# Kernel tuning notes

Measured on AMD Instinct MI355X. Metric: run time of the kernel, lower is better.

## Reference

```python
import jax, jax.numpy as jnp
import numpy as np

B, S, D, H = 2, 2048, 1024, 16
DH = D // H
DFF = 4 * D
EPS = 1e-5


def layer_norm(x, w, b):
    m = jnp.mean(x, axis=-1, keepdims=True)
    v = jnp.mean((x - m) ** 2, axis=-1, keepdims=True)
    return (x - m) / jnp.sqrt(v + EPS) * w + b


def setup_inputs() -> dict:
    key = jax.random.key(0)
    ks = jax.random.split(key, 12)
    s = 0.02
    x = jax.random.normal(ks[0], (B, S, D), dtype=jnp.float32)
    mask = jnp.tril(jnp.ones((S, S), dtype=jnp.int32))  # causal mask, 0 = blocked
    Wq = jax.random.normal(ks[1], (H, D, DH), dtype=jnp.float32) * s
    Wk = jax.random.normal(ks[2], (H, D, DH), dtype=jnp.float32) * s
    Wv = jax.random.normal(ks[3], (H, D, DH), dtype=jnp.float32) * s
    Wo = jax.random.normal(ks[4], (D, D), dtype=jnp.float32) * s
    bo = jnp.zeros((D,), dtype=jnp.float32)
    W1 = jax.random.normal(ks[5], (D, DFF), dtype=jnp.float32) * s
    b1 = jnp.zeros((DFF,), dtype=jnp.float32)
    W2 = jax.random.normal(ks[6], (DFF, D), dtype=jnp.float32) * s
    b2 = jnp.zeros((D,), dtype=jnp.float32)
    ln1_w = jnp.ones((D,), dtype=jnp.float32)
    ln1_b = jnp.zeros((D,), dtype=jnp.float32)
    ln2_w = jnp.ones((D,), dtype=jnp.float32)
    ln2_b = jnp.zeros((D,), dtype=jnp.float32)
    return {"x": x, "mask": mask, "Wq": Wq, "Wk": Wk, "Wv": Wv, "Wo": Wo,
            "bo": bo, "W1": W1, "b1": b1, "W2": W2, "b2": b2,
            "ln1_w": ln1_w, "ln1_b": ln1_b, "ln2_w": ln2_w, "ln2_b": ln2_b}


def reference(x, mask, Wq, Wk, Wv, Wo, bo, W1, b1, W2, b2,
              ln1_w, ln1_b, ln2_w, ln2_b):
    # --- pre-LN attention ---
    xn = layer_norm(x, ln1_w, ln1_b)
    q = jnp.einsum('bsd,hdk->bhsk', xn, Wq)  # [B,H,S,DH]
    k = jnp.einsum('bsd,hdk->bhsk', xn, Wk)
    v = jnp.einsum('bsd,hdk->bhsk', xn, Wv)
    scores = jnp.einsum('bhik,bhjk->bhij', q, k) / jnp.sqrt(jnp.float32(DH))
    scores = jnp.where(mask == 0, jnp.float32(-1e9), scores)  # mask broadcasts [S,S]->[B,H,S,S]
    attn = jax.nn.softmax(scores, axis=-1)
    o = jnp.einsum('bhij,bhjk->bhik', attn, v)        # [B,H,S,DH]
    o = o.transpose(0, 2, 1, 3).reshape(x.shape[0], x.shape[1], D)  # concat heads
    attn_out = o @ Wo + bo
    x = x + attn_out
    # --- pre-LN FFN ---
    xn2 = layer_norm(x, ln2_w, ln2_b)
    h = jax.nn.relu(xn2 @ W1 + b1)
    x = x + (h @ W2 + b2)
    return x
```

## Files before the change

kernel.cpp:

```cpp
#include <hip/hip_runtime.h>
#include <hip/hip_bf16.h>
#include <stdint.h>

#define DEV static __device__ __forceinline__

using f32x4  = __attribute__((ext_vector_type(4))) float;
using bf16x8 = __attribute__((ext_vector_type(8))) __bf16;

constexpr int SEQ = 2048;

DEV unsigned short f2bf(float f) {
  union { float f; unsigned u; } c; c.f = f;
  unsigned u = c.u;
  u += 0x7fffu + ((u >> 16) & 1u);
  return (unsigned short)(u >> 16);
}

DEV float wred_sum(float v) {
  #pragma unroll
  for (int m = 32; m > 0; m >>= 1) v += __shfl_xor(v, m, 64);
  return v;
}

DEV void g2l16(const unsigned short* g, unsigned short* l) {
  __builtin_amdgcn_global_load_lds(
      (const __attribute__((address_space(1))) void*)g,
      (__attribute__((address_space(3))) void*)l, 16, 0, 0);
}

DEV int xcd_map(int bid, int nwg) {
  const int cpx = nwg >> 3;
  return (bid & 7) * cpx + (bid >> 3);
}

__global__ __launch_bounds__(256) void convw_kernel(
    const float* __restrict__ in, unsigned short* __restrict__ out,
    int K, int Nh)
{
  const int h = blockIdx.z;
  const float* inh = in + (size_t)h * K * Nh;
  unsigned short* outh = out + (size_t)h * Nh * K;
  const int n0 = blockIdx.x * 32, k0 = blockIdx.y * 32;
  __shared__ float t[32][33];
  const int tx = threadIdx.x & 31, ty = threadIdx.x >> 5;
  #pragma unroll
  for (int r = 0; r < 32; r += 8)
    t[ty + r][tx] = inh[(size_t)(k0 + ty + r) * Nh + (n0 + tx)];
  __syncthreads();
  #pragma unroll
  for (int r = 0; r < 32; r += 8)
    outh[(size_t)(n0 + ty + r) * K + (k0 + tx)] = f2bf(t[tx][ty + r]);
}

__global__ __launch_bounds__(256) void ln_kernel(
    const float* __restrict__ x, const float* __restrict__ w,
    const float* __restrict__ b, unsigned short* __restrict__ out)
{
  const int row = blockIdx.x;
  const int tid = threadIdx.x;
  const float4 v = ((const float4*)(x + (size_t)row * 1024))[tid];
  float s  = v.x + v.y + v.z + v.w;
  float s2 = v.x*v.x + v.y*v.y + v.z*v.z + v.w*v.w;
  s = wred_sum(s); s2 = wred_sum(s2);
  __shared__ float rs[4], rs2[4];
  const int wave = tid >> 6, lane = tid & 63;
  if (lane == 0) { rs[wave] = s; rs2[wave] = s2; }
  __syncthreads();
  const float S  = rs[0] + rs[1] + rs[2] + rs[3];
  const float S2 = rs2[0] + rs2[1] + rs2[2] + rs2[3];
  const float mean = S * (1.f / 1024.f);
  const float var  = S2 * (1.f / 1024.f) - mean * mean;
  const float inv  = rsqrtf(var + 1e-5f);
  const float4 wv = ((const float4*)w)[tid];
  const float4 bv = ((const float4*)b)[tid];
  ushort4 o;
  o.x = f2bf((v.x - mean) * inv * wv.x + bv.x);
  o.y = f2bf((v.y - mean) * inv * wv.y + bv.y);
  o.z = f2bf((v.z - mean) * inv * wv.z + bv.z);
  o.w = f2bf((v.w - mean) * inv * wv.w + bv.w);
  ((ushort4*)(out + (size_t)row * 1024))[tid] = o;
}

template<int EPI>
__global__ __launch_bounds__(256) void gemm_kp(
    const unsigned short* __restrict__ A, const unsigned short* __restrict__ BT,
    void* __restrict__ Cout, const float* __restrict__ bias,
    const float* __restrict__ res, int M, int N, int K)
{
  __shared__ unsigned short sA[4][128 * 32];
  __shared__ unsigned short sB[4][64 * 32];
  const int tid = threadIdx.x;
  const int wave = tid >> 6, lane = tid & 63;
  const int wr = wave >> 1, wc = wave & 1;
  const int bid = xcd_map(blockIdx.y * gridDim.x + blockIdx.x, gridDim.x * gridDim.y);
  const int m0 = (bid / gridDim.x) * 128, n0 = (bid % gridDim.x) * 64;
  const int lr = lane & 15, lg = lane >> 4;
  const int wb = tid & 192;

  const f32x4 zero = {0.f, 0.f, 0.f, 0.f};
  f32x4 acc[4][2];
  #pragma unroll
  for (int i = 0; i < 4; ++i)
    #pragma unroll
    for (int j = 0; j < 2; ++j) acc[i][j] = zero;

  auto STAGE = [&](int slot, int kt) {
    const int k0 = kt * 32;
    #pragma unroll
    for (int r = 0; r < 2; ++r) {
      const int c = tid + 256 * r;
      const int row = c >> 2;
      const int so = ((c & 3) ^ ((row >> 1) & 3)) * 8;
      g2l16(A + (size_t)(m0 + row) * K + k0 + so, sA[slot] + (size_t)(r * 256 + wb) * 8);
    }
    const int row = tid >> 2;
    const int so = ((tid & 3) ^ ((row >> 1) & 3)) * 8;
    g2l16(BT + (size_t)(n0 + row) * K + k0 + so, sB[slot] + (size_t)wb * 8);
  };

  const int nt = K / 32;
  STAGE(0, 0); STAGE(1, 1); STAGE(2, 2);

  for (int t = 0; t < nt; ++t) {
    asm volatile("s_waitcnt vmcnt(6)" ::: "memory");
    __builtin_amdgcn_s_barrier();
    const int slot = t & 3;
    bf16x8 af[4], bfr[2];
    #pragma unroll
    for (int i = 0; i < 4; ++i) {
      const int row = wr * 64 + i * 16 + lr;
      af[i] = *(const bf16x8*)(sA[slot] + row * 32 + ((lg ^ ((row >> 1) & 3)) << 3));
    }
    #pragma unroll
    for (int j = 0; j < 2; ++j) {
      const int row = wc * 32 + j * 16 + lr;
      bfr[j] = *(const bf16x8*)(sB[slot] + row * 32 + ((lg ^ ((row >> 1) & 3)) << 3));
    }
    #pragma unroll
    for (int i = 0; i < 4; ++i)
      #pragma unroll
      for (int j = 0; j < 2; ++j)
        acc[i][j] = __builtin_amdgcn_mfma_f32_16x16x32_bf16(af[i], bfr[j], acc[i][j], 0, 0, 0);
    const int nx = (t + 3 < nt) ? t + 3 : nt - 1;
    STAGE((t + 3) & 3, nx);
  }
  asm volatile("s_waitcnt vmcnt(0)" ::: "memory");

  #pragma unroll
  for (int i = 0; i < 4; ++i) {
    #pragma unroll
    for (int j = 0; j < 2; ++j) {
      #pragma unroll
      for (int r = 0; r < 4; ++r) {
        const int row = m0 + wr * 64 + i * 16 + lg * 4 + r;
        const int col = n0 + wc * 32 + j * 16 + lr;
        const float v = acc[i][j][r];
        if (EPI == 1) {
          ((float*)Cout)[(size_t)row * N + col] = v + bias[col] + res[(size_t)row * N + col];
        } else {
          ((unsigned short*)Cout)[(size_t)row * N + col] = f2bf(v);
        }
      }
    }
  }
}

template<int EPI>
__global__ __launch_bounds__(512) void gemm256(
    const unsigned short* __restrict__ A, const unsigned short* __restrict__ BT,
    void* __restrict__ Cout, const float* __restrict__ bias,
    int M, int N, int K)
{
  __shared__ unsigned short sA[2][256 * 64];
  __shared__ unsigned short sB[2][256 * 64];
  const int tid = threadIdx.x;
  const int lane = tid & 63;
  const int wave = tid >> 6;
  const int wm = wave >> 2, wn = wave & 3;
  const int bid = xcd_map(blockIdx.y * gridDim.x + blockIdx.x, gridDim.x * gridDim.y);
  const int m0 = (bid / gridDim.x) * 256, n0 = (bid % gridDim.x) * 256;
  const int lr = lane & 15, lg = lane >> 4;

  const f32x4 zero = {0.f, 0.f, 0.f, 0.f};
  f32x4 acc[8][4];
  #pragma unroll
  for (int i = 0; i < 8; ++i)
    #pragma unroll
    for (int j = 0; j < 4; ++j) acc[i][j] = zero;

  auto STAGE = [&](int buf, int k0) {
    #pragma unroll
    for (int r = 0; r < 4; ++r) {
      const int c = tid + 512 * r;
      const int row = c >> 3;
      const int slot = (c & 7) ^ (row & 7);
      const int cb = (tid & 448) + 512 * r;
      g2l16(A  + (size_t)(m0 + row) * K + k0 + slot * 8, sA[buf] + (size_t)cb * 8);
      g2l16(BT + (size_t)(n0 + row) * K + k0 + slot * 8, sB[buf] + (size_t)cb * 8);
    }
  };
  auto RD = [&](const unsigned short* base, int R, int C) -> const bf16x8* {
    return (const bf16x8*)(base + R * 64 + ((((C >> 3) ^ (R & 7))) << 3));
  };

  const int nt = K / 64;
  STAGE(0, 0);
  asm volatile("s_waitcnt vmcnt(0)" ::: "memory");
  __syncthreads();

  for (int t = 0; t < nt; ++t) {
    const int buf = t & 1;
    if (t + 1 < nt) STAGE(buf ^ 1, (t + 1) * 64);
    #pragma unroll
    for (int p = 0; p < 4; ++p) {
      const int ih = p >> 1, jh = p & 1;
      bf16x8 af[4][2], bfr[2][2];
      #pragma unroll
      for (int i = 0; i < 4; ++i)
        #pragma unroll
        for (int kk = 0; kk < 2; ++kk)
          af[i][kk] = *RD(sA[buf], wm * 128 + (ih * 4 + i) * 16 + lr, kk * 32 + lg * 8);
      #pragma unroll
      for (int j = 0; j < 2; ++j)
        #pragma unroll
        for (int kk = 0; kk < 2; ++kk)
          bfr[j][kk] = *RD(sB[buf], wn * 64 + (jh * 2 + j) * 16 + lr, kk * 32 + lg * 8);
      __builtin_amdgcn_s_setprio(1);
      #pragma unroll
      for (int i = 0; i < 4; ++i)
        #pragma unroll
        for (int j = 0; j < 2; ++j)
          #pragma unroll
          for (int kk = 0; kk < 2; ++kk)
            acc[ih * 4 + i][jh * 2 + j] = __builtin_amdgcn_mfma_f32_16x16x32_bf16(
                af[i][kk], bfr[j][kk], acc[ih * 4 + i][jh * 2 + j], 0, 0, 0);
      __builtin_amdgcn_s_setprio(0);
      if (p < 3) __builtin_amdgcn_s_barrier();
    }
    asm volatile("s_waitcnt vmcnt(0)" ::: "memory");
    __builtin_amdgcn_s_barrier();
  }

  #pragma unroll
  for (int i = 0; i < 8; ++i) {
    #pragma unroll
    for (int j = 0; j < 4; ++j) {
      #pragma unroll
      for (int r = 0; r < 4; ++r) {
        const int row = m0 + wm * 128 + i * 16 + lg * 4 + r;
        const int col = n0 + wn * 64 + j * 16 + lr;
        const float v = acc[i][j][r];
        if (EPI == 0) {
          ((unsigned short*)Cout)[(size_t)row * N + col] = f2bf(v);
        } else {
          float t2 = v + bias[col];
          t2 = t2 > 0.f ? t2 : 0.f;
          ((unsigned short*)Cout)[(size_t)row * N + col] = f2bf(t2);
        }
      }
    }
  }
}

constexpr int PAD  = 72;
constexpr int VPAD = 136;

__global__ __launch_bounds__(256) void attn_mfma(
    const unsigned short* __restrict__ qkv, unsigned short* __restrict__ o)
{
  const int p  = blockIdx.x >> 5;
  const int bh = blockIdx.x & 31;
  const int b = bh >> 4, h = bh & 15;
  const int tid = threadIdx.x;
  const int wave = tid >> 6, lane = tid & 63;
  const int lr = lane & 15, lg = lane >> 4;
  const float SC = 0.125f * 1.44269504089f;

  __shared__ unsigned short Ks[128 * PAD];
  __shared__ unsigned short Vs[64 * VPAD];
  __shared__ unsigned short Ps[4][16 * VPAD];

  #pragma unroll 1
  for (int ph = 0; ph < 2; ++ph) {
    const int qi = ph ? (31 - p) : p;
    const int q0 = qi * 64;

    const size_t qbase = ((size_t)(b * SEQ + q0 + wave * 16 + lr)) * 3072 + h * 64;
    bf16x8 qb[2];
    qb[0] = *(const bf16x8*)(qkv + qbase + lg * 8);
    qb[1] = *(const bf16x8*)(qkv + qbase + 32 + lg * 8);

    const f32x4 zero = {0.f, 0.f, 0.f, 0.f};
    f32x4 o_acc[4];
    #pragma unroll
    for (int dn = 0; dn < 4; ++dn) o_acc[dn] = zero;
    float m_run = -1e30f, l_run = 0.f;

    const int ntiles = (qi + 2) >> 1;
    for (int t = 0; t < ntiles; ++t) {
      const int j0 = t * 128;
      __syncthreads();
      #pragma unroll
      for (int r = 0; r < 4; ++r) {
        const int c = tid + 256 * r;
        const int row = c >> 3, seg = c & 7;
        const size_t base = ((size_t)(b * SEQ + j0 + row)) * 3072 + 1024 + h * 64 + seg * 8;
        *(int4*)(Ks + row * PAD + seg * 8) = *(const int4*)(qkv + base);
      }
      #pragma unroll
      for (int r = 0; r < 4; ++r) {
        const int c = tid + 256 * r;
        const int key = c & 127, dseg = c >> 7;
        const size_t base = ((size_t)(b * SEQ + j0 + key)) * 3072 + 2048 + h * 64 + dseg * 8;
        int4 rv = *(const int4*)(qkv + base);
        const unsigned short* u = (const unsigned short*)&rv;
        #pragma unroll
        for (int e = 0; e < 8; ++e) Vs[(dseg * 8 + e) * VPAD + key] = u[e];
      }
      __syncthreads();

      f32x4 s[8];
      __builtin_amdgcn_s_setprio(1);
      #pragma unroll
      for (int n = 0; n < 8; ++n) {
        const bf16x8 kf0 = *(const bf16x8*)(Ks + (n * 16 + lr) * PAD + lg * 8);
        const bf16x8 kf1 = *(const bf16x8*)(Ks + (n * 16 + lr) * PAD + 32 + lg * 8);
        s[n] = __builtin_amdgcn_mfma_f32_16x16x32_bf16(kf0, qb[0], zero, 0, 0, 0);
        s[n] = __builtin_amdgcn_mfma_f32_16x16x32_bf16(kf1, qb[1], s[n], 0, 0, 0);
      }
      __builtin_amdgcn_s_setprio(0);

      const bool diag = (t == ntiles - 1);
      const int q = q0 + wave * 16 + lr;
      const int kbase = j0 + lg * 4;
      float zm = -3e38f;
      #pragma unroll
      for (int n = 0; n < 8; ++n)
        #pragma unroll
        for (int r = 0; r < 4; ++r) {
          float z = s[n][r] * SC;
          if (diag && (kbase + n * 16 + r > q)) z = -3e38f;
          s[n][r] = z;
          zm = fmaxf(zm, z);
        }
      zm = fmaxf(zm, __shfl_xor(zm, 16, 64));
      zm = fmaxf(zm, __shfl_xor(zm, 32, 64));
      const float mnew = fmaxf(m_run, zm);
      const float alpha = exp2f(m_run - mnew);
      m_run = mnew;
      float psum = 0.f;
      #pragma unroll
      for (int n = 0; n < 8; ++n) {
        ushort4 w;
        float p0 = exp2f(s[n][0] - mnew); psum += p0; w.x = f2bf(p0);
        float p1 = exp2f(s[n][1] - mnew); psum += p1; w.y = f2bf(p1);
        float p2 = exp2f(s[n][2] - mnew); psum += p2; w.z = f2bf(p2);
        float p3 = exp2f(s[n][3] - mnew); psum += p3; w.w = f2bf(p3);
        *(ushort4*)(&Ps[wave][lr * VPAD + n * 16 + lg * 4]) = w;
      }
      psum += __shfl_xor(psum, 16, 64);
      psum += __shfl_xor(psum, 32, 64);
      l_run = l_run * alpha + psum;

      float a4[4];
      #pragma unroll
      for (int r = 0; r < 4; ++r) a4[r] = __shfl(alpha, lg * 4 + r, 64);
      #pragma unroll
      for (int dn = 0; dn < 4; ++dn)
        #pragma unroll
        for (int r = 0; r < 4; ++r) o_acc[dn][r] *= a4[r];

      bf16x8 pa[4];
      #pragma unroll
      for (int kk = 0; kk < 4; ++kk)
        pa[kk] = *(const bf16x8*)(&Ps[wave][lr * VPAD + kk * 32 + lg * 8]);
      __builtin_amdgcn_s_setprio(1);
      #pragma unroll
      for (int dn = 0; dn < 4; ++dn) {
        #pragma unroll
        for (int kk = 0; kk < 4; ++kk) {
          const bf16x8 vf = *(const bf16x8*)(Vs + (dn * 16 + lr) * VPAD + kk * 32 + lg * 8);
          o_acc[dn] = __builtin_amdgcn_mfma_f32_16x16x32_bf16(pa[kk], vf, o_acc[dn], 0, 0, 0);
        }
      }
      __builtin_amdgcn_s_setprio(0);
    }

    float linv[4];
    #pragma unroll
    for (int r = 0; r < 4; ++r) linv[r] = 1.f / __shfl(l_run, lg * 4 + r, 64);
    #pragma unroll
    for (int r = 0; r < 4; ++r) {
      const int qq = q0 + wave * 16 + lg * 4 + r;
      const size_t obase = ((size_t)(b * SEQ + qq)) * 1024 + h * 64;
      #pragma unroll
      for (int dn = 0; dn < 4; ++dn)
        o[obase + dn * 16 + lr] = f2bf(o_acc[dn][r] * linv[r]);
    }
  }
}

extern "C" void kernel_launch(void* const* d_in, const int* in_sizes, int n_in,
                              void* d_out, int out_size, void* d_ws, size_t ws_size,
                              hipStream_t stream) {
  const float* x    = (const float*)d_in[0];
  const float* Wq   = (const float*)d_in[2];
  const float* Wk   = (const float*)d_in[3];
  const float* Wv   = (const float*)d_in[4];
  const float* Wo   = (const float*)d_in[5];
  const float* bo   = (const float*)d_in[6];
  const float* W1   = (const float*)d_in[7];
  const float* b1   = (const float*)d_in[8];
  const float* W2   = (const float*)d_in[9];
  const float* b2   = (const float*)d_in[10];
  const float* ln1w = (const float*)d_in[11];
  const float* ln1b = (const float*)d_in[12];
  const float* ln2w = (const float*)d_in[13];
  const float* ln2b = (const float*)d_in[14];

  char* ws = (char*)d_ws;
  unsigned short* WqkvT = (unsigned short*)(ws);
  unsigned short* WoT   = (unsigned short*)(ws + 6291456);
  unsigned short* W1T   = (unsigned short*)(ws + 8388608);
  unsigned short* W2T   = (unsigned short*)(ws + 16777216);
  unsigned short* xn    = (unsigned short*)(ws + 25165824);
  float*          x1    = (float*)        (ws + 33554432);
  unsigned short* qkv   = (unsigned short*)(ws + 50331648);
  unsigned short* oc    = (unsigned short*)(ws + 75497472);
  unsigned short* hbuf  = qkv;

  convw_kernel<<<dim3(2, 32, 16),  256, 0, stream>>>(Wq, WqkvT,               1024, 64);
  convw_kernel<<<dim3(2, 32, 16),  256, 0, stream>>>(Wk, WqkvT + 1024 * 1024, 1024, 64);
  convw_kernel<<<dim3(2, 32, 16),  256, 0, stream>>>(Wv, WqkvT + 2048 * 1024, 1024, 64);
  convw_kernel<<<dim3(32, 32, 1),  256, 0, stream>>>(Wo, WoT, 1024, 1024);
  convw_kernel<<<dim3(128, 32, 1), 256, 0, stream>>>(W1, W1T, 1024, 4096);
  convw_kernel<<<dim3(32, 128, 1), 256, 0, stream>>>(W2, W2T, 4096, 1024);

  ln_kernel<<<4096, 256, 0, stream>>>(x, ln1w, ln1b, xn);
  gemm256<0><<<dim3(12, 16), 512, 0, stream>>>(xn, WqkvT, qkv, nullptr, 4096, 3072, 1024);
  attn_mfma<<<512, 256, 0, stream>>>(qkv, oc);
  gemm_kp<1><<<dim3(16, 32), 256, 0, stream>>>(oc, WoT, x1, bo, x, 4096, 1024, 1024);
  ln_kernel<<<4096, 256, 0, stream>>>(x1, ln2w, ln2b, xn);
  gemm256<2><<<dim3(16, 16), 512, 0, stream>>>(xn, W1T, hbuf, b1, 4096, 4096, 1024);
  gemm_kp<1><<<dim3(16, 32), 256, 0, stream>>>(hbuf, W2T, (float*)d_out, b2, x1, 4096, 1024, 4096);
}
```

Measured before the change: 245.3 us.

## Process paired causal query tiles concurrently in attention, sharing K/V tile loads

The attention kernel now runs 512 threads per block. Two groups of four waves handle the long and short causal query tiles (31-p and p) at the same time instead of one after the other. Both groups share each K/V tile load into LDS, and the short group idles once its tiles run out. K is staged with a direct global-to-LDS copy into an XOR-swizzled layout instead of a padded one. The softmax scale is folded into the Q columns of the QKV GEMM epilogue, and P is converted with native bf16 casts. This removes duplicate K/V traffic and serial phases, at the cost of higher register/LDS pressure per block and idle waves in the short group.

```diff
diff --git a/kernel.cpp b/kernel.cpp
--- a/kernel.cpp
+++ b/kernel.cpp
@@ -5,6 +5,7 @@
 #define DEV static __device__ __forceinline__
 
 using f32x4  = __attribute__((ext_vector_type(4))) float;
+using bf16x4 = __attribute__((ext_vector_type(4))) __bf16;
 using bf16x8 = __attribute__((ext_vector_type(8))) __bf16;
 
 constexpr int SEQ = 2048;
@@ -249,8 +250,9 @@
       for (int r = 0; r < 4; ++r) {
         const int row = m0 + wm * 128 + i * 16 + lg * 4 + r;
         const int col = n0 + wn * 64 + j * 16 + lr;
-        const float v = acc[i][j][r];
+        float v = acc[i][j][r];
         if (EPI == 0) {
+          if (col < 1024) v *= 0.18033688f;
           ((unsigned short*)Cout)[(size_t)row * N + col] = f2bf(v);
         } else {
           float t2 = v + bias[col];
@@ -262,10 +264,9 @@
   }
 }
 
-constexpr int PAD  = 72;
 constexpr int VPAD = 136;
 
-__global__ __launch_bounds__(256) void attn_mfma(
+__global__ __launch_bounds__(512) void attn_mfma(
     const unsigned short* __restrict__ qkv, unsigned short* __restrict__ o)
 {
   const int p  = blockIdx.x >> 5;
@@ -273,72 +274,74 @@
   const int b = bh >> 4, h = bh & 15;
   const int tid = threadIdx.x;
   const int wave = tid >> 6, lane = tid & 63;
+  const int grp = wave >> 2, wv = wave & 3;
   const int lr = lane & 15, lg = lane >> 4;
-  const float SC = 0.125f * 1.44269504089f;
-
-  __shared__ unsigned short Ks[128 * PAD];
+
+  const int qi = grp ? p : (31 - p);
+  const int mynt = (qi >> 1) + 1;
+  const int nt_long = ((31 - p) >> 1) + 1;
+  const int q0 = qi * 64;
+
+  __shared__ unsigned short Ks[128 * 64];
   __shared__ unsigned short Vs[64 * VPAD];
-  __shared__ unsigned short Ps[4][16 * VPAD];
-
-  #pragma unroll 1
-  for (int ph = 0; ph < 2; ++ph) {
-    const int qi = ph ? (31 - p) : p;
-    const int q0 = qi * 64;
-
-    const size_t qbase = ((size_t)(b * SEQ + q0 + wave * 16 + lr)) * 3072 + h * 64;
-    bf16x8 qb[2];
-    qb[0] = *(const bf16x8*)(qkv + qbase + lg * 8);
-    qb[1] = *(const bf16x8*)(qkv + qbase + 32 + lg * 8);
-
-    const f32x4 zero = {0.f, 0.f, 0.f, 0.f};
-    f32x4 o_acc[4];
-    #pragma unroll
-    for (int dn = 0; dn < 4; ++dn) o_acc[dn] = zero;
-    float m_run = -1e30f, l_run = 0.f;
-
-    const int ntiles = (qi + 2) >> 1;
-    for (int t = 0; t < ntiles; ++t) {
-      const int j0 = t * 128;
-      __syncthreads();
-      #pragma unroll
-      for (int r = 0; r < 4; ++r) {
-        const int c = tid + 256 * r;
-        const int row = c >> 3, seg = c & 7;
-        const size_t base = ((size_t)(b * SEQ + j0 + row)) * 3072 + 1024 + h * 64 + seg * 8;
-        *(int4*)(Ks + row * PAD + seg * 8) = *(const int4*)(qkv + base);
-      }
-      #pragma unroll
-      for (int r = 0; r < 4; ++r) {
-        const int c = tid + 256 * r;
-        const int key = c & 127, dseg = c >> 7;
-        const size_t base = ((size_t)(b * SEQ + j0 + key)) * 3072 + 2048 + h * 64 + dseg * 8;
-        int4 rv = *(const int4*)(qkv + base);
-        const unsigned short* u = (const unsigned short*)&rv;
-        #pragma unroll
-        for (int e = 0; e < 8; ++e) Vs[(dseg * 8 + e) * VPAD + key] = u[e];
-      }
-      __syncthreads();
-
+  __shared__ unsigned short Ps[8][16 * VPAD];
+
+  const size_t qbase = ((size_t)(b * SEQ + q0 + wv * 16 + lr)) * 3072 + h * 64;
+  bf16x8 qb[2];
+  qb[0] = *(const bf16x8*)(qkv + qbase + lg * 8);
+  qb[1] = *(const bf16x8*)(qkv + qbase + 32 + lg * 8);
+
+  const f32x4 zero = {0.f, 0.f, 0.f, 0.f};
+  f32x4 o_acc[4];
+  #pragma unroll
+  for (int dn = 0; dn < 4; ++dn) o_acc[dn] = zero;
+  float m_run = -1e30f, l_run = 0.f;
+
+  for (int t = 0; t < nt_long; ++t) {
+    const int j0 = t * 128;
+    __syncthreads();
+    #pragma unroll
+    for (int r = 0; r < 2; ++r) {
+      const int c = tid + 512 * r;
+      const int row = c >> 3;
+      const int slot = (c & 7) ^ (row & 7);
+      const size_t gsrc = ((size_t)(b * SEQ + j0 + row)) * 3072 + 1024 + h * 64 + slot * 8;
+      g2l16(qkv + gsrc, Ks + (size_t)((tid & 448) + 512 * r) * 8);
+    }
+    #pragma unroll
+    for (int r = 0; r < 2; ++r) {
+      const int c = tid + 512 * r;
+      const int key = c & 127, dseg = c >> 7;
+      const size_t base = ((size_t)(b * SEQ + j0 + key)) * 3072 + 2048 + h * 64 + dseg * 8;
+      int4 rv = *(const int4*)(qkv + base);
+      const unsigned short* u = (const unsigned short*)&rv;
+      #pragma unroll
+      for (int e = 0; e < 8; ++e) Vs[(dseg * 8 + e) * VPAD + key] = u[e];
+    }
+    __syncthreads();
+
+    if (t < mynt) {
       f32x4 s[8];
       __builtin_amdgcn_s_setprio(1);
       #pragma unroll
       for (int n = 0; n < 8; ++n) {
-        const bf16x8 kf0 = *(const bf16x8*)(Ks + (n * 16 + lr) * PAD + lg * 8);
-        const bf16x8 kf1 = *(const bf16x8*)(Ks + (n * 16 + lr) * PAD + 32 + lg * 8);
+        const int row = n * 16 + lr;
+        const bf16x8 kf0 = *(const bf16x8*)(Ks + row * 64 + ((lg ^ (row & 7)) << 3));
+        const bf16x8 kf1 = *(const bf16x8*)(Ks + row * 64 + (((4 + lg) ^ (row & 7)) << 3));
         s[n] = __builtin_amdgcn_mfma_f32_16x16x32_bf16(kf0, qb[0], zero, 0, 0, 0);
         s[n] = __builtin_amdgcn_mfma_f32_16x16x32_bf16(kf1, qb[1], s[n], 0, 0, 0);
       }
       __builtin_amdgcn_s_setprio(0);
 
-      const bool diag = (t == ntiles - 1);
-      const int q = q0 + wave * 16 + lr;
+      const bool diag = (t == mynt - 1);
+      const int q = q0 + wv * 16 + lr;
       const int kbase = j0 + lg * 4;
       float zm = -3e38f;
       #pragma unroll
       for (int n = 0; n < 8; ++n)
         #pragma unroll
         for (int r = 0; r < 4; ++r) {
-          float z = s[n][r] * SC;
+          float z = s[n][r];
           if (diag && (kbase + n * 16 + r > q)) z = -3e38f;
           s[n][r] = z;
           zm = fmaxf(zm, z);
@@ -351,12 +354,12 @@
       float psum = 0.f;
       #pragma unroll
       for (int n = 0; n < 8; ++n) {
-        ushort4 w;
-        float p0 = exp2f(s[n][0] - mnew); psum += p0; w.x = f2bf(p0);
-        float p1 = exp2f(s[n][1] - mnew); psum += p1; w.y = f2bf(p1);
-        float p2 = exp2f(s[n][2] - mnew); psum += p2; w.z = f2bf(p2);
-        float p3 = exp2f(s[n][3] - mnew); psum += p3; w.w = f2bf(p3);
-        *(ushort4*)(&Ps[wave][lr * VPAD + n * 16 + lg * 4]) = w;
+        float p0 = exp2f(s[n][0] - mnew); psum += p0;
+        float p1 = exp2f(s[n][1] - mnew); psum += p1;
+        float p2 = exp2f(s[n][2] - mnew); psum += p2;
+        float p3 = exp2f(s[n][3] - mnew); psum += p3;
+        bf16x4 pw = { (__bf16)p0, (__bf16)p1, (__bf16)p2, (__bf16)p3 };
+        *(bf16x4*)(&Ps[wave][lr * VPAD + n * 16 + lg * 4]) = pw;
       }
       psum += __shfl_xor(psum, 16, 64);
       psum += __shfl_xor(psum, 32, 64);
@@ -385,18 +388,18 @@
       }
       __builtin_amdgcn_s_setprio(0);
     }
-
-    float linv[4];
-    #pragma unroll
-    for (int r = 0; r < 4; ++r) linv[r] = 1.f / __shfl(l_run, lg * 4 + r, 64);
-    #pragma unroll
-    for (int r = 0; r < 4; ++r) {
-      const int qq = q0 + wave * 16 + lg * 4 + r;
-      const size_t obase = ((size_t)(b * SEQ + qq)) * 1024 + h * 64;
-      #pragma unroll
-      for (int dn = 0; dn < 4; ++dn)
-        o[obase + dn * 16 + lr] = f2bf(o_acc[dn][r] * linv[r]);
-    }
+  }
+
+  float linv[4];
+  #pragma unroll
+  for (int r = 0; r < 4; ++r) linv[r] = 1.f / __shfl(l_run, lg * 4 + r, 64);
+  #pragma unroll
+  for (int r = 0; r < 4; ++r) {
+    const int qq = q0 + wv * 16 + lg * 4 + r;
+    const size_t obase = ((size_t)(b * SEQ + qq)) * 1024 + h * 64;
+    #pragma unroll
+    for (int dn = 0; dn < 4; ++dn)
+      o[obase + dn * 16 + lr] = f2bf(o_acc[dn][r] * linv[r]);
   }
 }
 
@@ -438,7 +441,7 @@
 
   ln_kernel<<<4096, 256, 0, stream>>>(x, ln1w, ln1b, xn);
   gemm256<0><<<dim3(12, 16), 512, 0, stream>>>(xn, WqkvT, qkv, nullptr, 4096, 3072, 1024);
-  attn_mfma<<<512, 256, 0, stream>>>(qkv, oc);
+  attn_mfma<<<512, 512, 0, stream>>>(qkv, oc);
   gemm_kp<1><<<dim3(16, 32), 256, 0, stream>>>(oc, WoT, x1, bo, x, 4096, 1024, 1024);
   ln_kernel<<<4096, 256, 0, stream>>>(x1, ln2w, ln2b, xn);
   gemm256<2><<<dim3(16, 16), 512, 0, stream>>>(xn, W1T, hbuf, b1, 4096, 4096, 1024);
```

Result: no change. 243.4 us (-0.8%).
